# Kernel optimization log

Hardware: AMD Instinct MI355X
Metric: run time of the kernel (lower is better)

## Reference

```python
import jax, jax.numpy as jnp
import numpy as np

NUM_LAYERS = 5  # shared parameters across layers


def _crelu(z):
    # complex ReLU: ReLU applied independently to real and imag parts
    return jnp.maximum(z.real, 0.0) + 1j * jnp.maximum(z.imag, 0.0)


def _layer(Habs2, diagH, noise, maxpow, v, ar, dl, rc):
    # ---- u step ----
    # cov: [B,K,1] = |H|^2 @ |v|^2 (sum over last dim keepdim is identity for width-1) + noise
    cov = jnp.sum(Habs2 @ (jnp.abs(v) ** 2), axis=-1, keepdims=True) + noise[..., None]
    u = diagH[..., None] * v / cov  # [B,K,1] complex
    # ---- w step ---- (w_poly=None branch)
    err = 1.0 - jnp.conj(u) * diagH[..., None] * v
    w = 1.0 / err  # [B,K,1] complex
    # ---- v step ----
    v_tilde = jnp.conj(diagH)[..., None] * u * w  # [B,K,1]
    ul = (jnp.abs(u) ** 2) * jnp.abs(w)  # real [B,K,1]
    ul = jnp.sum(jnp.abs(jnp.swapaxes(Habs2, -2, -1) @ ul), axis=-1, keepdims=True)
    mu = jnp.maximum(jnp.abs(v_tilde) / jnp.sqrt(maxpow)[..., None] - ul, 0.0)
    ula = (ul + mu).astype(v_tilde.dtype)
    # ar + diagload branches: [B,K,1,1] @ [1,C] -> [B,K,1,C]
    vt = (v_tilde / ula)[..., None] @ ar + v_tilde[..., None] @ dl
    # nonlin + recombination: [B,K,1,C] @ [C,1] -> [B,K,1,1]
    vt = _crelu(vt) @ rc
    v_new = vt[..., 0]  # [B,K,1]
    # power correction
    cur = jnp.maximum(maxpow[..., None], jnp.abs(v_new) ** 2)
    corr = jnp.minimum(jnp.sqrt(maxpow[..., None] / cur), 1.0)
    return v_new * corr, u, w


def setup_inputs() -> dict:
    key = jax.random.key(0)
    ks = jax.random.split(key, 12)
    B, K, C = 64, 512, 4
    s = 1.0 / np.sqrt(C + 1)
    inp = {
        "h_re": jax.random.normal(ks[0], (B, K, K), jnp.float32),
        "h_im": jax.random.normal(ks[1], (B, K, K), jnp.float32),
        "user_noise_pow": jax.random.uniform(ks[2], (B, K), jnp.float32, 0.1, 1.0),
        "bss_maxpow": jnp.ones((B, K), jnp.float32),
        "v_in_re": jax.random.normal(ks[3], (B, K, 1), jnp.float32) * 0.5,
        "v_in_im": jax.random.normal(ks[4], (B, K, 1), jnp.float32) * 0.5,
        "ar_re": jax.random.normal(ks[5], (1, C), jnp.float32) * s,
        "ar_im": jax.random.normal(ks[6], (1, C), jnp.float32) * s,
        "dl_re": jax.random.normal(ks[7], (1, C), jnp.float32) * s,
        "dl_im": jax.random.normal(ks[8], (1, C), jnp.float32) * s,
        "rc_re": jax.random.normal(ks[9], (C, 1), jnp.float32) * s,
        "rc_im": jax.random.normal(ks[10], (C, 1), jnp.float32) * s,
    }
    return inp


def reference(h_re, h_im, user_noise_pow, bss_maxpow, v_in_re, v_in_im,
              ar_re, ar_im, dl_re, dl_im, rc_re, rc_im):
    H = (h_re + 1j * h_im).astype(jnp.complex64)
    Habs2 = h_re * h_re + h_im * h_im  # |H|^2, real [B,K,K]
    diagH = jnp.diagonal(H, axis1=-2, axis2=-1)  # [B,K]
    v = (v_in_re + 1j * v_in_im).astype(jnp.complex64)
    ar = (ar_re + 1j * ar_im).astype(jnp.complex64)
    dl = (dl_re + 1j * dl_im).astype(jnp.complex64)
    rc = (rc_re + 1j * rc_im).astype(jnp.complex64)
    vs = []
    for _ in range(NUM_LAYERS):
        v, u, w = _layer(Habs2, diagH, user_noise_pow, bss_maxpow, v, ar, dl, rc)
        vs.append(v)
    vstack = jnp.stack(vs, 0)  # [L,B,K,1] complex
    # return real/imag stacked so the output is a real tensor: [L,B,K,1,2]
    return jnp.stack([vstack.real, vstack.imag], axis=-1)
```

## Files before the change

### kernel.cpp

```cpp
#include <hip/hip_runtime.h>

#define B    64
#define K    512
#define C    4
#define NL   5
#define BK   (B*K)
#define ROWS 128
#define NT   1024
#define GRID (B*4)

typedef _Float16 half_t;
typedef _Float16 half8 __attribute__((ext_vector_type(8)));
typedef float    f4    __attribute__((ext_vector_type(4)));

#define HABS_BYTES (ROWS*K*2)
#define VST_OFF    (HABS_BYTES)
#define PART_OFF   (VST_OFF + K*8)
#define XSQ_OFF    (PART_OFF + 8*K*4)
#define DAB_OFF    (XSQ_OFF + K*4)
#define MPL_OFF    (DAB_OFF + ROWS*4)
#define NZ_OFF     (MPL_OFF + K*4)
#define SMEM_BYTES (NZ_OFF + ROWS*4)

__device__ __forceinline__ void quartet_barrier(unsigned* qb) {
    __syncthreads();
    if (threadIdx.x == 0) {
        unsigned g = __hip_atomic_load(qb + 1, __ATOMIC_RELAXED,
                                       __HIP_MEMORY_SCOPE_AGENT);
        unsigned a = __hip_atomic_fetch_add(qb, 1u, __ATOMIC_ACQ_REL,
                                            __HIP_MEMORY_SCOPE_AGENT);
        if (a == 3u) {
            __hip_atomic_store(qb, 0u, __ATOMIC_RELAXED,
                               __HIP_MEMORY_SCOPE_AGENT);
            __hip_atomic_store(qb + 1, g + 1u, __ATOMIC_RELEASE,
                               __HIP_MEMORY_SCOPE_AGENT);
        } else {
            while (__hip_atomic_load(qb + 1, __ATOMIC_RELAXED,
                                     __HIP_MEMORY_SCOPE_AGENT) == g)
                __builtin_amdgcn_s_sleep(2);
            __builtin_amdgcn_fence(__ATOMIC_ACQUIRE, "agent");
        }
    }
    __syncthreads();
}

__global__ __launch_bounds__(NT, 4) void k_all(
    const float* __restrict__ hre,  const float* __restrict__ him,
    const float* __restrict__ noise,const float* __restrict__ mp,
    const float* __restrict__ vre,  const float* __restrict__ vim,
    const float* __restrict__ ar_re,const float* __restrict__ ar_im,
    const float* __restrict__ dl_re,const float* __restrict__ dl_im,
    const float* __restrict__ rc_re,const float* __restrict__ rc_im,
    float2* __restrict__ vtilde,
    float*  __restrict__ ulpart,
    unsigned* __restrict__ bar,
    float* __restrict__ out)
{
    extern __shared__ char smem[];
    half_t* habs = (half_t*)smem;
    float2* vst  = (float2*)(smem + VST_OFF);
    float*  part = (float*) (smem + PART_OFF);
    float*  xsq  = (float*) (smem + XSQ_OFF);
    float*  dab  = (float*) (smem + DAB_OFF);
    float*  mpl  = (float*) (smem + MPL_OFF);
    float*  nz   = (float*) (smem + NZ_OFF);

    const int tid  = threadIdx.x;
    const int lane = tid & 63;
    const int w    = tid >> 6;
    const int b    = blockIdx.x & 63;
    const int q    = blockIdx.x >> 6;
    const int j0   = q * ROWS;
    unsigned* qb   = bar + ((unsigned)b << 5);

    {
        const size_t gb = ((size_t)b * K + j0) * K;
        const f4* rp = (const f4*)(hre + gb);
        const f4* ip = (const f4*)(him + gb);
        f4 lr0[2], lr1[2], li0[2], li1[2];
        lr0[0] = __builtin_nontemporal_load(rp + tid * 2);
        lr1[0] = __builtin_nontemporal_load(rp + tid * 2 + 1);
        li0[0] = __builtin_nontemporal_load(ip + tid * 2);
        li1[0] = __builtin_nontemporal_load(ip + tid * 2 + 1);
#pragma unroll
        for (int i = 0; i < 8; ++i) {
            const int cur = i & 1, nxt = cur ^ 1;
            if (i < 7) {
                const int e4 = (i + 1) * (NT * 2) + tid * 2;
                lr0[nxt] = __builtin_nontemporal_load(rp + e4);
                lr1[nxt] = __builtin_nontemporal_load(rp + e4 + 1);
                li0[nxt] = __builtin_nontemporal_load(ip + e4);
                li1[nxt] = __builtin_nontemporal_load(ip + e4 + 1);
            }
            const f4 r0 = lr0[cur], r1 = lr1[cur];
            const f4 m0 = li0[cur], m1 = li1[cur];
            float s[8];
            s[0] = r0.x*r0.x + m0.x*m0.x; s[1] = r0.y*r0.y + m0.y*m0.y;
            s[2] = r0.z*r0.z + m0.z*m0.z; s[3] = r0.w*r0.w + m0.w*m0.w;
            s[4] = r1.x*r1.x + m1.x*m1.x; s[5] = r1.y*r1.y + m1.y*m1.y;
            s[6] = r1.z*r1.z + m1.z*m1.z; s[7] = r1.w*r1.w + m1.w*m1.w;
            half8 hh;
#pragma unroll
            for (int t = 0; t < 8; ++t) hh[t] = (_Float16)s[t];
            const int e = i * (NT * 8) + tid * 8;
            *(half8*)(habs + e) = hh;
            const int row  = e >> 9;
            const int col0 = e & (K - 1);
            const int j    = j0 + row;
            if (j >= col0 && j < col0 + 8) dab[row] = s[j - col0];
        }
        if (tid < K) {
            float a = vre[b * K + tid], c = vim[b * K + tid];
            vst[tid] = make_float2(a, c);
            xsq[tid] = a * a + c * c;
            mpl[tid] = mp[b * K + tid];
        } else if (tid < K + ROWS) {
            nz[tid - K] = noise[b * K + j0 + (tid - K)];
        }
    }
    __syncthreads();

    int buf = 0;
    for (int l = 0; l < NL; ++l) {
        const f4 xa = ((const f4*)xsq)[lane * 2];
        const f4 xb = ((const f4*)xsq)[lane * 2 + 1];
        half8 h[8];
        float rs[8];
#pragma unroll
        for (int r = 0; r < 8; ++r) {
            h[r] = *(const half8*)(habs + ((w * 8 + r) * K + lane * 8));
            float acc = (float)h[r][0]*xa.x + (float)h[r][1]*xa.y +
                        (float)h[r][2]*xa.z + (float)h[r][3]*xa.w +
                        (float)h[r][4]*xb.x + (float)h[r][5]*xb.y +
                        (float)h[r][6]*xb.z + (float)h[r][7]*xb.w;
#pragma unroll
            for (int off = 32; off; off >>= 1) acc += __shfl_xor(acc, off, 64);
            rs[r] = acc;
        }
        float ulv_own = 0.f;
        if (lane < 8) {
            const int row = w * 8 + lane;
            const int j   = j0 + row;
            const int bj  = b * K + j;
            float s = lane==0?rs[0]:lane==1?rs[1]:lane==2?rs[2]:lane==3?rs[3]:
                      lane==4?rs[4]:lane==5?rs[5]:lane==6?rs[6]:rs[7];
            const float cov = s + nz[row];
            const float d2  = dab[row];
            const float A   = d2 * xsq[j];
            const float ww  = cov / (cov - A);
            const float sc  = d2 * ww / cov;
            const float2 vv = vst[j];
            vtilde[buf * BK + bj] = make_float2(sc * vv.x, sc * vv.y);
            ulv_own = A * ww / (cov * cov);
        }
        float ulv[8];
#pragma unroll
        for (int r = 0; r < 8; ++r) ulv[r] = __shfl(ulv_own, r, 64);

        float pw[8];
#pragma unroll
        for (int t = 0; t < 8; ++t) {
            pw[t] = (float)h[0][t]*ulv[0] + (float)h[1][t]*ulv[1] +
                    (float)h[2][t]*ulv[2] + (float)h[3][t]*ulv[3] +
                    (float)h[4][t]*ulv[4] + (float)h[5][t]*ulv[5] +
                    (float)h[6][t]*ulv[6] + (float)h[7][t]*ulv[7];
        }
        float* pr = part + (w & 7) * K + lane * 8;
        if (w < 8) {
#pragma unroll
            for (int t = 0; t < 8; ++t) pr[t] = pw[t];
        }
        __syncthreads();
        if (w >= 8) {
#pragma unroll
            for (int t = 0; t < 8; ++t) pr[t] += pw[t];
        }
        __syncthreads();
        if (tid < K) {
            float s2 = part[tid]       + part[K + tid]   + part[2*K + tid] +
                       part[3*K + tid] + part[4*K + tid] + part[5*K + tid] +
                       part[6*K + tid] + part[7*K + tid];
            ulpart[(size_t)buf * (B*4*K) + ((size_t)(b*4 + q)) * K + tid] = s2;
        }
        quartet_barrier(qb);

        if (tid < K) {
            const int k  = tid;
            const int bk = b * K + k;
            const float* up = ulpart + (size_t)buf * (B*4*K) + (size_t)(b*4) * K;
            float ul = up[k] + up[K + k] + up[2*K + k] + up[3*K + k];
            const float2 vt = vtilde[buf * BK + bk];
            const float p   = mpl[k];
            const float avt = sqrtf(vt.x*vt.x + vt.y*vt.y);
            const float mu  = fmaxf(avt / sqrtf(p) - ul, 0.f);
            const float inv = 1.f / (ul + mu);
            float ax = 0.f, ay = 0.f;
#pragma unroll
            for (int c = 0; c < C; ++c) {
                const float gre = ar_re[c] * inv + dl_re[c];
                const float gim = ar_im[c] * inv + dl_im[c];
                float zre = vt.x * gre - vt.y * gim;
                float zim = vt.x * gim + vt.y * gre;
                zre = fmaxf(zre, 0.f);
                zim = fmaxf(zim, 0.f);
                ax += zre * rc_re[c] - zim * rc_im[c];
                ay += zre * rc_im[c] + zim * rc_re[c];
            }
            const float n2   = ax*ax + ay*ay;
            const float cur  = fmaxf(p, n2);
            const float corr = fminf(sqrtf(p / cur), 1.f);
            ax *= corr; ay *= corr;
            if ((k >> 7) == q)
                ((float2*)out)[(size_t)l * BK + bk] = make_float2(ax, ay);
            vst[k] = make_float2(ax, ay);
            xsq[k] = ax * ax + ay * ay;
        }
        __syncthreads();
        buf ^= 1;
    }
}

extern "C" void kernel_launch(void* const* d_in, const int* in_sizes, int n_in,
                              void* d_out, int out_size, void* d_ws, size_t ws_size,
                              hipStream_t stream) {
    const float* hre   = (const float*)d_in[0];
    const float* him   = (const float*)d_in[1];
    const float* noise = (const float*)d_in[2];
    const float* mp    = (const float*)d_in[3];
    const float* vre   = (const float*)d_in[4];
    const float* vim   = (const float*)d_in[5];
    const float* ar_re = (const float*)d_in[6];
    const float* ar_im = (const float*)d_in[7];
    const float* dl_re = (const float*)d_in[8];
    const float* dl_im = (const float*)d_in[9];
    const float* rc_re = (const float*)d_in[10];
    const float* rc_im = (const float*)d_in[11];
    float* out = (float*)d_out;

    char*     ws     = (char*)d_ws;
    float2*   vtilde = (float2*)ws;
    float*    ulpart = (float*)(ws + 2*(size_t)BK*8);
    unsigned* bar    = (unsigned*)(ws + 2*(size_t)BK*8 + 2*(size_t)B*4*K*4);

    static bool attr_done = false;
    if (!attr_done) {
        hipFuncSetAttribute((const void*)k_all,
                            hipFuncAttributeMaxDynamicSharedMemorySize,
                            SMEM_BYTES);
        attr_done = true;
    }

    hipMemsetAsync(bar, 0, B * 32 * sizeof(unsigned), stream);

    hipLaunchKernelGGL(k_all, dim3(GRID), dim3(NT), SMEM_BYTES, stream,
                       hre, him, noise, mp, vre, vim,
                       ar_re, ar_im, dl_re, dl_im, rc_re, rc_im,
                       vtilde, ulpart, bar, out);
}
```

Before: 221.2 us.

## Use monotonic quartet barrier with relaxed agent-scope loads and stores for exchange

Replaces the reset-and-generation quartet barrier with a single monotonically increasing counter that each block increments and then polls against a per-layer target. The acquire/release fences are dropped; the cross-block vtilde and ulpart exchange now uses relaxed agent-scope atomic loads and stores instead. Each block also reuses its own partial sum from registers and reads only the three peer partials. The intent is to shorten the inter-block synchronisation and remove fence overhead on each of the five layers. The risk is that correctness now depends on the counter being zeroed before every launch and on relaxed atomics being enough for ordering without explicit fences.

```diff
diff --git a/kernel.cpp b/kernel.cpp
--- a/kernel.cpp
+++ b/kernel.cpp
@@ -22,24 +22,35 @@
 #define NZ_OFF     (MPL_OFF + K*4)
 #define SMEM_BYTES (NZ_OFF + ROWS*4)
 
-__device__ __forceinline__ void quartet_barrier(unsigned* qb) {
+__device__ __forceinline__ float ld_l3(const float* p) {
+    return __uint_as_float(__hip_atomic_load((const unsigned*)p,
+        __ATOMIC_RELAXED, __HIP_MEMORY_SCOPE_AGENT));
+}
+__device__ __forceinline__ void st_l3(float* p, float v) {
+    __hip_atomic_store((unsigned*)p, __float_as_uint(v),
+        __ATOMIC_RELAXED, __HIP_MEMORY_SCOPE_AGENT);
+}
+__device__ __forceinline__ void st_l3_2(float2* p, float2 v) {
+    unsigned long long u = ((unsigned long long)__float_as_uint(v.y) << 32)
+                         | (unsigned long long)__float_as_uint(v.x);
+    __hip_atomic_store((unsigned long long*)p, u,
+        __ATOMIC_RELAXED, __HIP_MEMORY_SCOPE_AGENT);
+}
+__device__ __forceinline__ float2 ld_l3_2(const float2* p) {
+    unsigned long long u = __hip_atomic_load((const unsigned long long*)p,
+        __ATOMIC_RELAXED, __HIP_MEMORY_SCOPE_AGENT);
+    return make_float2(__uint_as_float((unsigned)(u & 0xffffffffu)),
+                       __uint_as_float((unsigned)(u >> 32)));
+}
+
+__device__ __forceinline__ void quartet_barrier(unsigned* qb, unsigned target) {
     __syncthreads();
     if (threadIdx.x == 0) {
-        unsigned g = __hip_atomic_load(qb + 1, __ATOMIC_RELAXED,
-                                       __HIP_MEMORY_SCOPE_AGENT);
-        unsigned a = __hip_atomic_fetch_add(qb, 1u, __ATOMIC_ACQ_REL,
-                                            __HIP_MEMORY_SCOPE_AGENT);
-        if (a == 3u) {
-            __hip_atomic_store(qb, 0u, __ATOMIC_RELAXED,
+        __hip_atomic_fetch_add(qb, 1u, __ATOMIC_RELAXED,
                                __HIP_MEMORY_SCOPE_AGENT);
-            __hip_atomic_store(qb + 1, g + 1u, __ATOMIC_RELEASE,
-                               __HIP_MEMORY_SCOPE_AGENT);
-        } else {
-            while (__hip_atomic_load(qb + 1, __ATOMIC_RELAXED,
-                                     __HIP_MEMORY_SCOPE_AGENT) == g)
-                __builtin_amdgcn_s_sleep(2);
-            __builtin_amdgcn_fence(__ATOMIC_ACQUIRE, "agent");
-        }
+        while (__hip_atomic_load(qb, __ATOMIC_RELAXED,
+                                 __HIP_MEMORY_SCOPE_AGENT) < target)
+            __builtin_amdgcn_s_sleep(4);
     }
     __syncthreads();
 }
@@ -120,8 +131,8 @@
     }
     __syncthreads();
 
-    int buf = 0;
     for (int l = 0; l < NL; ++l) {
+        const int buf = l & 1;
         const f4 xa = ((const f4*)xsq)[lane * 2];
         const f4 xb = ((const f4*)xsq)[lane * 2 + 1];
         half8 h[8];
@@ -150,7 +161,7 @@
             const float ww  = cov / (cov - A);
             const float sc  = d2 * ww / cov;
             const float2 vv = vst[j];
-            vtilde[buf * BK + bj] = make_float2(sc * vv.x, sc * vv.y);
+            st_l3_2(&vtilde[buf * BK + bj], make_float2(sc * vv.x, sc * vv.y));
             ulv_own = A * ww / (cov * cov);
         }
         float ulv[8];
@@ -176,20 +187,25 @@
             for (int t = 0; t < 8; ++t) pr[t] += pw[t];
         }
         __syncthreads();
+        float s2 = 0.f;
         if (tid < K) {
-            float s2 = part[tid]       + part[K + tid]   + part[2*K + tid] +
-                       part[3*K + tid] + part[4*K + tid] + part[5*K + tid] +
-                       part[6*K + tid] + part[7*K + tid];
-            ulpart[(size_t)buf * (B*4*K) + ((size_t)(b*4 + q)) * K + tid] = s2;
-        }
-        quartet_barrier(qb);
+            s2 = part[tid]       + part[K + tid]   + part[2*K + tid] +
+                 part[3*K + tid] + part[4*K + tid] + part[5*K + tid] +
+                 part[6*K + tid] + part[7*K + tid];
+            st_l3(&ulpart[(size_t)buf * (B*4*K) + ((size_t)(b*4 + q)) * K + tid],
+                  s2);
+        }
+        quartet_barrier(qb, 4u * (unsigned)(l + 1));
 
         if (tid < K) {
             const int k  = tid;
             const int bk = b * K + k;
             const float* up = ulpart + (size_t)buf * (B*4*K) + (size_t)(b*4) * K;
-            float ul = up[k] + up[K + k] + up[2*K + k] + up[3*K + k];
-            const float2 vt = vtilde[buf * BK + bk];
+            float ul = s2;
+#pragma unroll
+            for (int qq = 0; qq < 4; ++qq)
+                if (qq != q) ul += ld_l3(up + qq * K + k);
+            const float2 vt = ld_l3_2(&vtilde[buf * BK + bk]);
             const float p   = mpl[k];
             const float avt = sqrtf(vt.x*vt.x + vt.y*vt.y);
             const float mu  = fmaxf(avt / sqrtf(p) - ul, 0.f);
@@ -216,7 +232,6 @@
             xsq[k] = ax * ax + ay * ay;
         }
         __syncthreads();
-        buf ^= 1;
     }
 }
 
```

Result: faster. 192.8 us (-12.9%).
